# Optimization experiments

Hardware: AMD Instinct MI355X
Metric: run time of the kernel (lower is better)

## Reference

```python
import jax, jax.numpy as jnp
import numpy as np

EMBED = 768
HEADS = 12
HEAD_DIM = EMBED // HEADS


def setup_inputs() -> dict:
    key = jax.random.key(0)
    ks = jax.random.split(key, 7)
    B, S = 4, 2048
    scale = 1.0 / np.sqrt(EMBED)
    return {
        "q": jax.random.normal(ks[0], (B, S, EMBED), dtype=jnp.float32),
        "k": jax.random.normal(ks[1], (B, S, EMBED), dtype=jnp.float32),
        "v": jax.random.normal(ks[2], (B, S, EMBED), dtype=jnp.float32),
        # NOTE: original torch code applies self.query to q, k AND v (bug kept faithfully),
        # so only the query projection and the output projection participate.
        "Wq": (jax.random.normal(ks[3], (EMBED, EMBED), dtype=jnp.float32) * scale),
        "bq": jnp.zeros((EMBED,), dtype=jnp.float32),
        "Wo": (jax.random.normal(ks[4], (EMBED, EMBED), dtype=jnp.float32) * scale),
        "bo": jnp.zeros((EMBED,), dtype=jnp.float32),
    }


def _split_heads(x):
    B, S, _ = x.shape
    return x.reshape(B, S, HEADS, HEAD_DIM).transpose(0, 2, 1, 3)  # [B,H,S,D]


def reference(q, k, v, Wq, bq, Wo, bo):
    # All three streams go through the *query* projection (faithful to source bug).
    qh = _split_heads(q @ Wq.T + bq)
    kh = _split_heads(k @ Wq.T + bq)
    vh = _split_heads(v @ Wq.T + bq)
    scores = jnp.einsum("bhsd,bhtd->bhst", qh, kh) / np.sqrt(HEAD_DIM)  # [B,H,S,S]
    attn = jax.nn.softmax(scores, axis=-1)  # dropout = identity (eval mode)
    out = jnp.einsum("bhst,bhtd->bhsd", attn, vh)  # [B,H,S,D]
    B, H, S, D = out.shape
    out = out.transpose(0, 2, 1, 3).reshape(B, S, H * D)  # [B,S,E]
    return out @ Wo.T + bo
```

## Files before the change

### kernel.cpp

```cpp
#include <hip/hip_runtime.h>

typedef unsigned int  uint32;
typedef unsigned short ushort_t;

using s16x8 = __attribute__((ext_vector_type(8))) short;
using bf8v  = __attribute__((ext_vector_type(8))) __bf16;
using f16x4 = __attribute__((ext_vector_type(4))) _Float16;
using f16x8 = __attribute__((ext_vector_type(8))) _Float16;
using f32x4 = __attribute__((ext_vector_type(4))) float;

typedef __attribute__((address_space(1))) void as1_void;
typedef __attribute__((address_space(3))) void as3_void;

__device__ __forceinline__ void gld16(const void* g, void* l) {
  __builtin_amdgcn_global_load_lds((const as1_void*)g, (as3_void*)l, 16, 0, 0);
}

__device__ __forceinline__ f32x4 mfma32(s16x8 a, s16x8 b, f32x4 c) {
  return __builtin_amdgcn_mfma_f32_16x16x32_bf16(
      __builtin_bit_cast(bf8v, a), __builtin_bit_cast(bf8v, b), c, 0, 0, 0);
}
__device__ __forceinline__ f32x4 mfma32h(f16x8 a, f16x8 b, f32x4 c) {
  return __builtin_amdgcn_mfma_f32_16x16x32_f16(a, b, c, 0, 0, 0);
}

__device__ __forceinline__ ushort_t f2bf(float f) {
  uint32 u = __float_as_uint(f);
  u += 0x7FFFu + ((u >> 16) & 1u);
  return (ushort_t)(u >> 16);
}
__device__ __forceinline__ f16x4 exp_pack(f32x4 st) {
  float e0 = __builtin_amdgcn_exp2f(st[0]);
  float e1 = __builtin_amdgcn_exp2f(st[1]);
  float e2 = __builtin_amdgcn_exp2f(st[2]);
  float e3 = __builtin_amdgcn_exp2f(st[3]);
  uint2 u = {__builtin_bit_cast(uint32, __builtin_amdgcn_cvt_pkrtz(e0, e1)),
             __builtin_bit_cast(uint32, __builtin_amdgcn_cvt_pkrtz(e2, e3))};
  return __builtin_bit_cast(f16x4, u);
}

__global__ __launch_bounds__(256) void cvt_all(const float* __restrict__ q,
                                               const float* __restrict__ k,
                                               const float* __restrict__ v,
                                               const float* __restrict__ Wq,
                                               const float* __restrict__ Wo,
                                               ushort_t* qb, ushort_t* kb, ushort_t* vb,
                                               ushort_t* wqb, ushort_t* wob) {
  int i = blockIdx.x * 256 + threadIdx.x;
  const float* s; ushort_t* d; int off;
  if (i < 4718592) {
    int st = i / 1572864; off = i - st * 1572864;
    s = st == 0 ? q : (st == 1 ? k : v);
    d = st == 0 ? qb : (st == 1 ? kb : vb);
  } else {
    int j = i - 4718592; int st = j / 147456; off = j - st * 147456;
    s = st ? Wo : Wq; d = st ? wob : wqb;
  }
  float4 f = ((const float4*)s)[off];
  ushort4 o = {f2bf(f.x), f2bf(f.y), f2bf(f.z), f2bf(f.w)};
  ((ushort4*)d)[off] = o;
}

__device__ __forceinline__ void gemm_core(const ushort_t* __restrict__ A,
                                          const ushort_t* __restrict__ Bw,
                                          ushort_t* As, ushort_t* Bs,
                                          int m0, int n0, f32x4 (&acc)[4][4]) {
  const int tid = threadIdx.x;
  const int wave = tid >> 6, lane = tid & 63;
  const int qd = lane >> 4, c = lane & 15;
  const int wm = wave >> 1, wn = wave & 1;
  const int pc0 = qd ^ (c & 7), pc1 = (4 + qd) ^ (c & 7);
  int row[4], cl[4], lb[4];
#pragma unroll
  for (int i = 0; i < 4; ++i) {
    int s = i * 256 + wave * 64 + lane;
    row[i] = s >> 3; cl[i] = (s & 7) ^ (row[i] & 7);
    lb[i] = (i * 256 + wave * 64) * 16;
  }
  for (int kt = 0; kt < 12; ++kt) {
    __syncthreads();
#pragma unroll
    for (int i = 0; i < 4; ++i) {
      gld16(A + (size_t)(m0 + row[i]) * 768 + kt * 64 + cl[i] * 8, (char*)As + lb[i]);
      gld16(Bw + (size_t)(n0 + row[i]) * 768 + kt * 64 + cl[i] * 8, (char*)Bs + lb[i]);
    }
    __syncthreads();
#pragma unroll
    for (int kk = 0; kk < 2; ++kk) {
      const int pcr = kk ? pc1 : pc0;
      s16x8 a[4], b[4];
#pragma unroll
      for (int i = 0; i < 4; ++i) a[i] = *(const s16x8*)(As + (wm * 64 + i * 16 + c) * 64 + pcr * 8);
#pragma unroll
      for (int j = 0; j < 4; ++j) b[j] = *(const s16x8*)(Bs + (wn * 64 + j * 16 + c) * 64 + pcr * 8);
#pragma unroll
      for (int i = 0; i < 4; ++i)
#pragma unroll
        for (int j = 0; j < 4; ++j) acc[i][j] = mfma32(a[i], b[j], acc[i][j]);
    }
  }
}

__global__ __launch_bounds__(256) void gemm_proj(const ushort_t* __restrict__ qb,
                                                 const ushort_t* __restrict__ kb,
                                                 const ushort_t* __restrict__ vb,
                                                 const ushort_t* __restrict__ Wqb,
                                                 const float* __restrict__ bias,
                                                 ushort_t* __restrict__ qh,
                                                 ushort_t* __restrict__ kh,
                                                 ushort_t* __restrict__ vt) {
  __shared__ __align__(16) ushort_t As[8192];
  __shared__ __align__(16) ushort_t Bs[8192];
  const int bz = blockIdx.z;
  const ushort_t* A = bz == 0 ? qb : (bz == 1 ? kb : vb);
  const int m0 = blockIdx.y * 128, n0 = blockIdx.x * 128;
  f32x4 acc[4][4] = {};
  gemm_core(A, Wqb, As, Bs, m0, n0, acc);
  const int tid = threadIdx.x, wave = tid >> 6, lane = tid & 63;
  const int qd = lane >> 4, c = lane & 15;
  const int wm = wave >> 1, wn = wave & 1;
  if (bz == 2) {
    const int sbase = m0 & 2047, bb = m0 >> 11;
#pragma unroll
    for (int p = 0; p < 2; ++p) {
      __syncthreads();
      if (wn == p) {
#pragma unroll
        for (int j = 0; j < 4; ++j) {
          int n64 = j * 16 + c;
          float bv = bias[n0 + p * 64 + n64];
#pragma unroll
          for (int i = 0; i < 4; ++i) {
            int ps8 = (wm * 16 + i * 4 + qd) ^ ((c & 7) << 2);
            uint2 w = {__builtin_bit_cast(uint32, __builtin_amdgcn_cvt_pkrtz(acc[i][j][0] + bv, acc[i][j][1] + bv)),
                       __builtin_bit_cast(uint32, __builtin_amdgcn_cvt_pkrtz(acc[i][j][2] + bv, acc[i][j][3] + bv))};
            *(uint2*)(As + n64 * 128 + ps8 * 4) = w;
          }
        }
      }
      __syncthreads();
      const int h = (n0 >> 6) + p;
#pragma unroll
      for (int e = 0; e < 4; ++e) {
        int ch = e * 256 + tid;
        int n64 = ch >> 4, u = ch & 15;
        uint4 w = *(const uint4*)(As + n64 * 128 + (u ^ ((n64 & 7) << 1)) * 8);
        *(uint4*)(vt + ((size_t)(bb * 12 + h) * 64 + n64) * 2048 + sbase + u * 8) = w;
      }
    }
  } else {
    ushort_t* dst = bz == 0 ? qh : kh;
    const float qsc = bz == 0 ? 0.18033688011112042f : 1.0f;
#pragma unroll
    for (int j = 0; j < 4; ++j) {
      int n = n0 + wn * 64 + j * 16 + c;
      float bv = bias[n];
      int h = n >> 6, d = n & 63;
#pragma unroll
      for (int i = 0; i < 4; ++i)
#pragma unroll
        for (int r = 0; r < 4; ++r) {
          int m = m0 + wm * 64 + i * 16 + qd * 4 + r;
          int bb = m >> 11, s = m & 2047;
          dst[((size_t)((bb * 12 + h) * 2048 + s)) * 64 + d] = f2bf((acc[i][j][r] + bv) * qsc);
        }
    }
  }
}

__global__ __launch_bounds__(256) void gemm_final(const ushort_t* __restrict__ A,
                                                  const ushort_t* __restrict__ Wob,
                                                  const float* __restrict__ bias,
                                                  float* __restrict__ out) {
  __shared__ __align__(16) ushort_t As[8192];
  __shared__ __align__(16) ushort_t Bs[8192];
  const int m0 = blockIdx.y * 128, n0 = blockIdx.x * 128;
  f32x4 acc[4][4] = {};
  gemm_core(A, Wob, As, Bs, m0, n0, acc);
  const int tid = threadIdx.x, wave = tid >> 6, lane = tid & 63;
  const int qd = lane >> 4, c = lane & 15;
  const int wm = wave >> 1, wn = wave & 1;
#pragma unroll
  for (int j = 0; j < 4; ++j) {
    int n = n0 + wn * 64 + j * 16 + c;
    float bv = bias[n];
#pragma unroll
    for (int i = 0; i < 4; ++i)
#pragma unroll
      for (int r = 0; r < 4; ++r) {
        int m = m0 + wm * 64 + i * 16 + qd * 4 + r;
        out[(size_t)m * 768 + n] = acc[i][j][r] + bv;
      }
  }
}

__global__ __launch_bounds__(256, 5) void flash(const ushort_t* __restrict__ qh,
                                                const ushort_t* __restrict__ kh,
                                                const ushort_t* __restrict__ vt,
                                                ushort_t* __restrict__ attn) {
  __shared__ __align__(16) ushort_t Ks[128 * 64];
  __shared__ __align__(16) ushort_t Vts[64 * 128];
  const int bid = blockIdx.x;
  const int bh = bid % 48, qt = bid / 48;
  const int tid = threadIdx.x, wave = tid >> 6, lane = tid & 63;
  const int qd = lane >> 4, c = lane & 15;
  const ushort_t* Qg = qh + (size_t)bh * 131072;
  const ushort_t* Kg = kh + (size_t)bh * 131072;
  const ushort_t* Vg = vt + (size_t)bh * 131072;
  const int sb = qt * 64 + wave * 16;

  s16x8 qf[2];
#pragma unroll
  for (int kk = 0; kk < 2; ++kk)
    qf[kk] = *(const s16x8*)(Qg + (size_t)(sb + c) * 64 + kk * 32 + qd * 8);

  const f32x4 z4 = {0.f, 0.f, 0.f, 0.f};
  const float FM = 12.0f;
  const f32x4 nFM = {-FM, -FM, -FM, -FM};
  f32x4 o[4], lacc = z4;
#pragma unroll
  for (int dn = 0; dn < 4; ++dn) o[dn] = z4;
  f16x8 ones8;
#pragma unroll
  for (int e = 0; e < 8; ++e) ones8[e] = (_Float16)1.f;

  const int kpc0 = (qd) ^ (c & 7);
  const int kpc1 = (4 + qd) ^ (c & 7);

  int kgrow[4], kcl[4], vrow[4], vcl[4], lbase[4];
#pragma unroll
  for (int i = 0; i < 4; ++i) {
    int s = i * 256 + wave * 64 + lane;
    int kr = s >> 3; kcl[i] = (s & 7) ^ (kr & 7);
    int u = kr & 31;
    kgrow[i] = (kr & ~31) | (((u >> 2) & 3) << 3) | (((u >> 4) & 1) << 2) | (u & 3);
    vrow[i] = s >> 4; vcl[i] = (s & 15) ^ (vrow[i] & 15);
    lbase[i] = (i * 256 + wave * 64) * 16;
  }

  for (int kt = 0; kt < 16; ++kt) {
    __syncthreads();
#pragma unroll
    for (int i = 0; i < 4; ++i)
      gld16(Kg + (size_t)(kt * 128 + kgrow[i]) * 64 + kcl[i] * 8, (char*)Ks + lbase[i]);
#pragma unroll
    for (int i = 0; i < 4; ++i)
      gld16(Vg + (size_t)vrow[i] * 2048 + kt * 128 + vcl[i] * 8, (char*)Vts + lbase[i]);
    __syncthreads();

#pragma unroll
    for (int p = 0; p < 4; ++p) {
      f16x4 p0[2];
#pragma unroll
      for (int tile = 0; tile < 2; ++tile) {
        const int r = (p * 2 + tile) * 16 + c;
        s16x8 a0 = *(const s16x8*)(Ks + r * 64 + kpc0 * 8);
        s16x8 a1 = *(const s16x8*)(Ks + r * 64 + kpc1 * 8);
        __builtin_amdgcn_s_setprio(1);
        f32x4 st0 = mfma32(a0, qf[0], nFM);
        st0 = mfma32(a1, qf[1], st0);
        __builtin_amdgcn_s_setprio(0);
        p0[tile] = exp_pack(st0);
      }
      f16x8 A0 = __builtin_shufflevector(p0[0], p0[1], 0, 1, 2, 3, 4, 5, 6, 7);
      __builtin_amdgcn_s_setprio(1);
      lacc = mfma32h(A0, ones8, lacc);
#pragma unroll
      for (int dn = 0; dn < 4; ++dn) {
        f16x8 vb = *(const f16x8*)(Vts + (dn * 16 + c) * 128 + ((4 * p + qd) ^ c) * 8);
        o[dn] = mfma32h(A0, vb, o[dn]);
      }
      __builtin_amdgcn_s_setprio(0);
    }
  }

  const int bb = bh / 12, h = bh % 12;
#pragma unroll
  for (int r = 0; r < 4; ++r) {
    float inv = 1.f / lacc[r];
    int s = sb + qd * 4 + r;
#pragma unroll
    for (int dn = 0; dn < 4; ++dn) {
      float val = o[dn][r] * inv;
      attn[((size_t)(bb * 2048 + s)) * 768 + h * 64 + dn * 16 + c] = f2bf(val);
    }
  }
}

extern "C" void kernel_launch(void* const* d_in, const int* in_sizes, int n_in,
                              void* d_out, int out_size, void* d_ws, size_t ws_size,
                              hipStream_t stream) {
  const float* q  = (const float*)d_in[0];
  const float* k  = (const float*)d_in[1];
  const float* v  = (const float*)d_in[2];
  const float* Wq = (const float*)d_in[3];
  const float* bq = (const float*)d_in[4];
  const float* Wo = (const float*)d_in[5];
  const float* bo = (const float*)d_in[6];
  float* out = (float*)d_out;
  char* ws = (char*)d_ws;

  ushort_t* qbf = (ushort_t*)(ws + 0);
  ushort_t* kbf = (ushort_t*)(ws + 12582912);
  ushort_t* vbf = (ushort_t*)(ws + 25165824);
  ushort_t* wqb = (ushort_t*)(ws + 37748736);
  ushort_t* wob = (ushort_t*)(ws + 38928384);
  ushort_t* qhp = (ushort_t*)(ws + 40108032);
  ushort_t* khp = (ushort_t*)(ws + 52690944);
  ushort_t* vtp = (ushort_t*)(ws + 65273856);
  ushort_t* att = (ushort_t*)(ws + 0);

  cvt_all<<<dim3(19584), 256, 0, stream>>>(q, k, v, Wq, Wo, qbf, kbf, vbf, wqb, wob);
  gemm_proj<<<dim3(6, 64, 3), 256, 0, stream>>>(qbf, kbf, vbf, wqb, bq, qhp, khp, vtp);
  flash<<<dim3(1536), 256, 0, stream>>>(qhp, khp, vtp, att);
  gemm_final<<<dim3(6, 64), 256, 0, stream>>>(att, wob, bo, out);
}
```

Measured before the change: 258.4 us.

## Double flash block to 512 threads and halve gemm_final M-tile to 64

The flash kernel now runs 8 waves per block covering 128 query rows, so each K/V tile staged in LDS is shared by twice as many waves and the number of blocks is halved. The final output GEMM gets its own loop with a 64x128 tile instead of the shared 128x128 core, doubling the grid to 768 blocks for better occupancy across CUs. The trade-off is more register pressure under the new launch bounds (512, 6) and lower per-block reuse in the output GEMM. Neither kernel double-buffers its loads.

```diff
diff --git a/kernel.cpp b/kernel.cpp
--- a/kernel.cpp
+++ b/kernel.cpp
@@ -172,29 +172,66 @@
                                                   const ushort_t* __restrict__ Wob,
                                                   const float* __restrict__ bias,
                                                   float* __restrict__ out) {
-  __shared__ __align__(16) ushort_t As[8192];
+  __shared__ __align__(16) ushort_t As[4096];
   __shared__ __align__(16) ushort_t Bs[8192];
-  const int m0 = blockIdx.y * 128, n0 = blockIdx.x * 128;
-  f32x4 acc[4][4] = {};
-  gemm_core(A, Wob, As, Bs, m0, n0, acc);
-  const int tid = threadIdx.x, wave = tid >> 6, lane = tid & 63;
+  const int m0 = blockIdx.y * 64, n0 = blockIdx.x * 128;
+  const int tid = threadIdx.x;
+  const int wave = tid >> 6, lane = tid & 63;
   const int qd = lane >> 4, c = lane & 15;
   const int wm = wave >> 1, wn = wave & 1;
+  const int pc0 = qd ^ (c & 7), pc1 = (4 + qd) ^ (c & 7);
+  f32x4 acc[2][4] = {};
+  int arow[2], acl[2], alb[2], brow[4], bcl[4], blb[4];
+#pragma unroll
+  for (int i = 0; i < 2; ++i) {
+    int s = i * 256 + tid;
+    arow[i] = s >> 3; acl[i] = (s & 7) ^ (arow[i] & 7);
+    alb[i] = (i * 256 + wave * 64) * 16;
+  }
+#pragma unroll
+  for (int i = 0; i < 4; ++i) {
+    int s = i * 256 + tid;
+    brow[i] = s >> 3; bcl[i] = (s & 7) ^ (brow[i] & 7);
+    blb[i] = (i * 256 + wave * 64) * 16;
+  }
+  for (int kt = 0; kt < 12; ++kt) {
+    __syncthreads();
+#pragma unroll
+    for (int i = 0; i < 2; ++i)
+      gld16(A + (size_t)(m0 + arow[i]) * 768 + kt * 64 + acl[i] * 8, (char*)As + alb[i]);
+#pragma unroll
+    for (int i = 0; i < 4; ++i)
+      gld16(Wob + (size_t)(n0 + brow[i]) * 768 + kt * 64 + bcl[i] * 8, (char*)Bs + blb[i]);
+    __syncthreads();
+#pragma unroll
+    for (int kk = 0; kk < 2; ++kk) {
+      const int pcr = kk ? pc1 : pc0;
+      s16x8 a[2], b[4];
+#pragma unroll
+      for (int i = 0; i < 2; ++i) a[i] = *(const s16x8*)(As + (wm * 32 + i * 16 + c) * 64 + pcr * 8);
+#pragma unroll
+      for (int j = 0; j < 4; ++j) b[j] = *(const s16x8*)(Bs + (wn * 64 + j * 16 + c) * 64 + pcr * 8);
+#pragma unroll
+      for (int i = 0; i < 2; ++i)
+#pragma unroll
+        for (int j = 0; j < 4; ++j) acc[i][j] = mfma32(a[i], b[j], acc[i][j]);
+    }
+  }
 #pragma unroll
   for (int j = 0; j < 4; ++j) {
     int n = n0 + wn * 64 + j * 16 + c;
     float bv = bias[n];
 #pragma unroll
-    for (int i = 0; i < 4; ++i)
+    for (int i = 0; i < 2; ++i)
 #pragma unroll
       for (int r = 0; r < 4; ++r) {
-        int m = m0 + wm * 64 + i * 16 + qd * 4 + r;
+        int m = m0 + wm * 32 + i * 16 + qd * 4 + r;
         out[(size_t)m * 768 + n] = acc[i][j][r] + bv;
       }
   }
 }
 
-__global__ __launch_bounds__(256, 5) void flash(const ushort_t* __restrict__ qh,
+__global__ __launch_bounds__(512, 6) void flash(const ushort_t* __restrict__ qh,
                                                 const ushort_t* __restrict__ kh,
                                                 const ushort_t* __restrict__ vt,
                                                 ushort_t* __restrict__ attn) {
@@ -207,7 +244,7 @@
   const ushort_t* Qg = qh + (size_t)bh * 131072;
   const ushort_t* Kg = kh + (size_t)bh * 131072;
   const ushort_t* Vg = vt + (size_t)bh * 131072;
-  const int sb = qt * 64 + wave * 16;
+  const int sb = qt * 128 + wave * 16;
 
   s16x8 qf[2];
 #pragma unroll
@@ -227,24 +264,24 @@
   const int kpc0 = (qd) ^ (c & 7);
   const int kpc1 = (4 + qd) ^ (c & 7);
 
-  int kgrow[4], kcl[4], vrow[4], vcl[4], lbase[4];
-#pragma unroll
-  for (int i = 0; i < 4; ++i) {
-    int s = i * 256 + wave * 64 + lane;
+  int kgrow[2], kcl[2], vrow[2], vcl[2], lbase[2];
+#pragma unroll
+  for (int i = 0; i < 2; ++i) {
+    int s = i * 512 + tid;
     int kr = s >> 3; kcl[i] = (s & 7) ^ (kr & 7);
     int u = kr & 31;
     kgrow[i] = (kr & ~31) | (((u >> 2) & 3) << 3) | (((u >> 4) & 1) << 2) | (u & 3);
     vrow[i] = s >> 4; vcl[i] = (s & 15) ^ (vrow[i] & 15);
-    lbase[i] = (i * 256 + wave * 64) * 16;
+    lbase[i] = (i * 512 + wave * 64) * 16;
   }
 
   for (int kt = 0; kt < 16; ++kt) {
     __syncthreads();
 #pragma unroll
-    for (int i = 0; i < 4; ++i)
+    for (int i = 0; i < 2; ++i)
       gld16(Kg + (size_t)(kt * 128 + kgrow[i]) * 64 + kcl[i] * 8, (char*)Ks + lbase[i]);
 #pragma unroll
-    for (int i = 0; i < 4; ++i)
+    for (int i = 0; i < 2; ++i)
       gld16(Vg + (size_t)vrow[i] * 2048 + kt * 128 + vcl[i] * 8, (char*)Vts + lbase[i]);
     __syncthreads();
 
@@ -312,6 +349,6 @@
 
   cvt_all<<<dim3(19584), 256, 0, stream>>>(q, k, v, Wq, Wo, qbf, kbf, vbf, wqb, wob);
   gemm_proj<<<dim3(6, 64, 3), 256, 0, stream>>>(qbf, kbf, vbf, wqb, bq, qhp, khp, vtp);
-  flash<<<dim3(1536), 256, 0, stream>>>(qhp, khp, vtp, att);
-  gemm_final<<<dim3(6, 64), 256, 0, stream>>>(att, wob, bo, out);
-}
+  flash<<<dim3(768), 512, 0, stream>>>(qhp, khp, vtp, att);
+  gemm_final<<<dim3(6, 128), 256, 0, stream>>>(att, wob, bo, out);
+}
```

New measurement: 251.6 us. -2.6%, faster.
